# Kernel optimization log

Hardware: AMD Instinct MI355X
Metric: run time of the kernel (lower is better)

## Reference

```python
import jax, jax.numpy as jnp
import numpy as np

NUM_GROUPS = 32
EPS = 1e-6


def group_norm(x, gamma, beta):
    # x: [b, c, h, w]
    b, c, h, w = x.shape
    xg = x.reshape(b, NUM_GROUPS, c // NUM_GROUPS, h, w)
    mean = jnp.mean(xg, axis=(2, 3, 4), keepdims=True)
    var = jnp.var(xg, axis=(2, 3, 4), keepdims=True)
    xn = ((xg - mean) * jax.lax.rsqrt(var + EPS)).reshape(b, c, h, w)
    return xn * gamma[None, :, None, None] + beta[None, :, None, None]


def conv1x1(x, w, b):
    # 1x1 conv == channel-mixing linear: x [b,c,h,w], w [o,c], b [o]
    return jnp.einsum('bchw,oc->bohw', x, w) + b[None, :, None, None]


def setup_inputs() -> dict:
    key = jax.random.key(0)
    ks = jax.random.split(key, 11)
    B, C, H, W = 4, 512, 64, 64
    scale = 1.0 / np.sqrt(C)
    inp = {
        'x': jax.random.normal(ks[0], (B, C, H, W), jnp.float32),
        'gn_gamma': jnp.ones((C,), jnp.float32),
        'gn_beta': jnp.zeros((C,), jnp.float32),
        'wq': jax.random.normal(ks[1], (C, C), jnp.float32) * scale,
        'bq': jnp.zeros((C,), jnp.float32),
        'wk': jax.random.normal(ks[2], (C, C), jnp.float32) * scale,
        'bk': jnp.zeros((C,), jnp.float32),
        'wv': jax.random.normal(ks[3], (C, C), jnp.float32) * scale,
        'bv': jnp.zeros((C,), jnp.float32),
        'wo': jax.random.normal(ks[4], (C, C), jnp.float32) * scale,
        'bo': jnp.zeros((C,), jnp.float32),
    }
    return inp


def reference(x, gn_gamma, gn_beta, wq, bq, wk, bk, wv, bv, wo, bo):
    b, c, h, w = x.shape
    nx = group_norm(x, gn_gamma, gn_beta)
    q = conv1x1(nx, wq, bq).reshape(b, c, h * w)
    k = conv1x1(nx, wk, bk).reshape(b, c, h * w)
    v = conv1x1(nx, wv, bv).reshape(b, c, h * w)
    # score[b, i, j] = <q[:, i], k[:, j]> / sqrt(c); softmax over j (keys)
    score = jnp.einsum('bci,bcj->bij', q, k) / jnp.sqrt(jnp.asarray(c, x.dtype))
    score = jax.nn.softmax(score, axis=2)
    # out[b, c, i] = sum_j v[b, c, j] * score[b, i, j]
    out = jnp.einsum('bcj,bij->bci', v, score).reshape(b, c, h, w)
    out = conv1x1(out, wo, bo)
    return x + out
```

## Files before the change

kernel.cpp:

```cpp
#include <hip/hip_runtime.h>

#define B_   4
#define C_   512
#define G_   32
#define CPG  16
#define N_   4096

typedef unsigned short u16;
typedef __attribute__((ext_vector_type(4))) float f32x4;
typedef __attribute__((ext_vector_type(8))) short s16x8;
typedef __attribute__((ext_vector_type(8))) u16   u16x8;
typedef __attribute__((ext_vector_type(4))) u16   u16x4;

__device__ __forceinline__ u16 f2bf(float f) {
    union { float f; unsigned u; } x; x.f = f;
    unsigned r = x.u + 0x7fffu + ((x.u >> 16) & 1u);
    return (u16)(r >> 16);
}

__global__ __launch_bounds__(256)
void gn_part_kernel(const float* __restrict__ x, float2* __restrict__ partial)
{
    int blk = blockIdx.x;
    int bg = blk >> 3, s = blk & 7;
    const float* base = x + (size_t)bg * CPG * N_ + s * 8192;
    int t = threadIdx.x;

    float sm = 0.f, ss = 0.f;
    #pragma unroll
    for (int i = 0; i < 8192; i += 1024) {
        float4 v = *reinterpret_cast<const float4*>(base + i + t * 4);
        sm += v.x + v.y + v.z + v.w;
        ss += v.x * v.x + v.y * v.y + v.z * v.z + v.w * v.w;
    }
    __shared__ float rs[256], rss[256];
    rs[t] = sm; rss[t] = ss;
    __syncthreads();
    for (int off = 128; off > 0; off >>= 1) {
        if (t < off) { rs[t] += rs[t + off]; rss[t] += rss[t + off]; }
        __syncthreads();
    }
    if (t == 0) partial[blk] = make_float2(rs[0], rss[0]);
}

__global__ __launch_bounds__(256)
void gn_combine_kernel(const float2* __restrict__ partial,
                       const float* __restrict__ gamma,
                       const float* __restrict__ beta,
                       float* __restrict__ scale, float* __restrict__ shift)
{
    int bg = threadIdx.x;
    if (bg >= 128) return;
    int b = bg >> 5, g = bg & 31;
    float sm = 0.f, ss = 0.f;
    #pragma unroll
    for (int s = 0; s < 8; ++s) {
        float2 p = partial[bg * 8 + s];
        sm += p.x; ss += p.y;
    }
    const float inv_n = 1.f / 65536.f;
    float mean = sm * inv_n;
    float var  = ss * inv_n - mean * mean;
    float rstd = rsqrtf(var + 1e-6f);
    #pragma unroll
    for (int cc = 0; cc < CPG; ++cc) {
        int c = g * CPG + cc;
        float sc = gamma[c] * rstd;
        scale[b * C_ + c] = sc;
        shift[b * C_ + c] = beta[c] - mean * sc;
    }
}

__global__ __launch_bounds__(256)
void wcvt_kernel(const float* __restrict__ wq, const float* __restrict__ wk,
                 const float* __restrict__ wv, const float* __restrict__ wo,
                 u16* __restrict__ wqb, u16* __restrict__ wkb,
                 u16* __restrict__ wvb, u16* __restrict__ wob)
{
    int idx = (blockIdx.x * 256 + threadIdx.x) * 4;
    {
        float4 a = *reinterpret_cast<const float4*>(wq + idx);
        u16x4 r = { f2bf(a.x), f2bf(a.y), f2bf(a.z), f2bf(a.w) };
        *reinterpret_cast<u16x4*>(wqb + idx) = r;
    }
    {
        float4 a = *reinterpret_cast<const float4*>(wk + idx);
        u16x4 r = { f2bf(a.x), f2bf(a.y), f2bf(a.z), f2bf(a.w) };
        *reinterpret_cast<u16x4*>(wkb + idx) = r;
    }
    {
        float4 a = *reinterpret_cast<const float4*>(wv + idx);
        u16x4 r = { f2bf(a.x), f2bf(a.y), f2bf(a.z), f2bf(a.w) };
        *reinterpret_cast<u16x4*>(wvb + idx) = r;
    }
    {
        float4 a = *reinterpret_cast<const float4*>(wo + idx);
        u16x4 r = { f2bf(a.x), f2bf(a.y), f2bf(a.z), f2bf(a.w) };
        *reinterpret_cast<u16x4*>(wob + idx) = r;
    }
}

__global__ __launch_bounds__(256)
void nxt_kernel(const float* __restrict__ x, const float* __restrict__ scale,
                const float* __restrict__ shift, u16* __restrict__ nx_t)
{
    int b  = blockIdx.z;
    int n0 = blockIdx.x * 64, c0 = blockIdx.y * 64;
    const float* xb = x + ((size_t)b * C_ + c0) * N_ + n0;
    u16* ob = nx_t + ((size_t)b * N_ + n0) * C_ + c0;
    int t = threadIdx.x;
    int tx = t & 15, ty = t >> 4;

    __shared__ float tile[64][65];
    #pragma unroll
    for (int r = 0; r < 4; ++r) {
        int c = ty * 4 + r;
        float sc = scale[b * C_ + c0 + c];
        float sh = shift[b * C_ + c0 + c];
        float4 v = *reinterpret_cast<const float4*>(xb + (size_t)c * N_ + tx * 4);
        tile[c][tx * 4 + 0] = v.x * sc + sh;
        tile[c][tx * 4 + 1] = v.y * sc + sh;
        tile[c][tx * 4 + 2] = v.z * sc + sh;
        tile[c][tx * 4 + 3] = v.w * sc + sh;
    }
    __syncthreads();
    int nn = t >> 2, cc0 = (t & 3) * 16;
    u16x8 o0, o1;
    #pragma unroll
    for (int j = 0; j < 8; ++j) o0[j] = f2bf(tile[cc0 + j][nn]);
    #pragma unroll
    for (int j = 0; j < 8; ++j) o1[j] = f2bf(tile[cc0 + 8 + j][nn]);
    *reinterpret_cast<u16x8*>(ob + (size_t)nn * C_ + cc0)     = o0;
    *reinterpret_cast<u16x8*>(ob + (size_t)nn * C_ + cc0 + 8) = o1;
}

template<int BM, int BN, int EPI>
__device__ __forceinline__
void gemm_dev(int i0, int j0,
              const u16* __restrict__ A, const u16* __restrict__ B,
              void* __restrict__ Dp, const float* __restrict__ bias,
              const float* __restrict__ resid,
              int Nn, int K, int lda, int ldb, float scl,
              float* __restrict__ psum, const float* __restrict__ colsc)
{
    constexpr int WM = BM / 2, WN = BN / 2;
    constexpr int MI = WM / 16, NI = WN / 16;

    __shared__ u16 As[BM * 64];
    __shared__ u16 Bs[BN * 64];

    const int t  = threadIdx.x;
    const int l  = t & 63;
    const int w  = t >> 6;
    const int wr = w >> 1;
    const int wc = w & 1;

    const int srow = l >> 3;
    const int sgr  = ((l & 7) ^ (l >> 3)) * 8;

    const int fr = l & 15;
    const int q  = l >> 4;

    f32x4 acc[MI][NI];
    #pragma unroll
    for (int a = 0; a < MI; ++a)
        #pragma unroll
        for (int b2 = 0; b2 < NI; ++b2) acc[a][b2] = 0.f;

    for (int k0 = 0; k0 < K; k0 += 64) {
        #pragma unroll
        for (int r = 0; r < BM / 32; ++r) {
            int s = r * 4 + w;
            const u16* ga = A + (size_t)(i0 + s * 8 + srow) * lda + (k0 + sgr);
            __builtin_amdgcn_global_load_lds(
                (const __attribute__((address_space(1))) void*)ga,
                (__attribute__((address_space(3))) void*)&As[s * 512], 16, 0, 0);
        }
        #pragma unroll
        for (int r = 0; r < BN / 32; ++r) {
            int s = r * 4 + w;
            const u16* gb = B + (size_t)(j0 + s * 8 + srow) * ldb + (k0 + sgr);
            __builtin_amdgcn_global_load_lds(
                (const __attribute__((address_space(1))) void*)gb,
                (__attribute__((address_space(3))) void*)&Bs[s * 512], 16, 0, 0);
        }
        __syncthreads();

        #pragma unroll
        for (int h = 0; h < 2; ++h) {
            s16x8 af[MI], bfr[NI];
            #pragma unroll
            for (int mi = 0; mi < MI; ++mi) {
                int r = wr * WM + mi * 16 + fr;
                int p = (h * 4 + q) ^ (r & 7);
                af[mi] = *reinterpret_cast<const s16x8*>(&As[r * 64 + p * 8]);
            }
            #pragma unroll
            for (int ni = 0; ni < NI; ++ni) {
                int r = wc * WN + ni * 16 + fr;
                int p = (h * 4 + q) ^ (r & 7);
                bfr[ni] = *reinterpret_cast<const s16x8*>(&Bs[r * 64 + p * 8]);
            }
            #pragma unroll
            for (int mi = 0; mi < MI; ++mi)
                #pragma unroll
                for (int ni = 0; ni < NI; ++ni)
                    acc[mi][ni] = __builtin_amdgcn_mfma_f32_16x16x32_bf16(
                        af[mi], bfr[ni], acc[mi][ni], 0, 0, 0);
        }
        __syncthreads();
    }

    const int orow = (l >> 4) * 4;
    const int ocol = l & 15;

    if constexpr (EPI == 2) {
        __shared__ float sstl[2][2][64];
        u16* D = (u16*)Dp;
        #pragma unroll
        for (int mi = 0; mi < MI; ++mi) {
            int ib = i0 + wr * WM + mi * 16 + orow;
            float pr[4] = {0.f, 0.f, 0.f, 0.f};
            #pragma unroll
            for (int ni = 0; ni < NI; ++ni) {
                int jb = j0 + wc * WN + ni * 16 + ocol;
                #pragma unroll
                for (int e = 0; e < 4; ++e) {
                    float ex = __expf(acc[mi][ni][e] * scl);
                    D[(size_t)(ib + e) * Nn + jb] = f2bf(ex);
                    pr[e] += ex;
                }
            }
            #pragma unroll
            for (int e = 0; e < 4; ++e) {
                pr[e] += __shfl_xor(pr[e], 1);
                pr[e] += __shfl_xor(pr[e], 2);
                pr[e] += __shfl_xor(pr[e], 4);
                pr[e] += __shfl_xor(pr[e], 8);
            }
            if ((l & 15) == 0) {
                #pragma unroll
                for (int e = 0; e < 4; ++e)
                    sstl[wr][wc][mi * 16 + (l >> 4) * 4 + e] = pr[e];
            }
        }
        __syncthreads();
        if (t < 128) {
            int wr2 = t >> 6, r = t & 63;
            psum[i0 + wr2 * 64 + r] = sstl[wr2][0][r] + sstl[wr2][1][r];
        }
    } else {
        #pragma unroll
        for (int mi = 0; mi < MI; ++mi) {
            #pragma unroll
            for (int ni = 0; ni < NI; ++ni) {
                int ib = i0 + wr * WM + mi * 16 + orow;
                int jb = j0 + wc * WN + ni * 16 + ocol;
                if constexpr (EPI == 0 || EPI == 1 || EPI == 4) {
                    u16* D = (u16*)Dp;
                    float bj = 0.f;
                    if constexpr (EPI == 0) bj = bias[jb];
                    #pragma unroll
                    for (int e = 0; e < 4; ++e) {
                        float vv = acc[mi][ni][e];
                        if constexpr (EPI == 0) vv += bj;
                        if constexpr (EPI == 1) vv += bias[ib + e];
                        D[(size_t)(ib + e) * Nn + jb] = f2bf(vv);
                    }
                } else {
                    float* D = (float*)Dp;
                    float cs = colsc[jb];
                    #pragma unroll
                    for (int e = 0; e < 4; ++e)
                        D[(size_t)(ib + e) * Nn + jb] =
                            acc[mi][ni][e] * cs + bias[ib + e] + resid[(size_t)(ib + e) * Nn + jb];
                }
            }
        }
    }
}

__global__ __launch_bounds__(256)
void qk_gemm(const u16* __restrict__ nx_t, const u16* __restrict__ wqb,
             const u16* __restrict__ wkb, const float* __restrict__ bq,
             const float* __restrict__ bk, u16* __restrict__ q_t,
             u16* __restrict__ k_t)
{
    int z = blockIdx.z, b = z & 3, isk = z >> 2;
    gemm_dev<128, 128, 0>(blockIdx.y * 128, blockIdx.x * 128,
                          nx_t + (size_t)b * N_ * C_, isk ? wkb : wqb,
                          (isk ? k_t : q_t) + (size_t)b * N_ * C_,
                          isk ? bk : bq, nullptr, C_, C_, C_, C_, 1.f,
                          nullptr, nullptr);
}

__global__ __launch_bounds__(256)
void v_gemm(const u16* __restrict__ wvb, const u16* __restrict__ nx_t,
            const float* __restrict__ bv, u16* __restrict__ vbuf)
{
    int b = blockIdx.z;
    gemm_dev<128, 128, 1>(blockIdx.y * 128, blockIdx.x * 128,
                          wvb, nx_t + (size_t)b * N_ * C_, vbuf + (size_t)b * C_ * N_,
                          bv, nullptr, N_, C_, C_, C_, 1.f, nullptr, nullptr);
}

__global__ __launch_bounds__(256)
void scores_gemm(const u16* __restrict__ q_t, const u16* __restrict__ k_t,
                 u16* __restrict__ S_bf, float* __restrict__ psum)
{
    int b = blockIdx.z;
    float* ps = psum + ((size_t)b * 32 + blockIdx.x) * N_;
    gemm_dev<128, 128, 2>(blockIdx.y * 128, blockIdx.x * 128,
                          q_t + (size_t)b * N_ * C_, k_t + (size_t)b * N_ * C_,
                          S_bf + (size_t)b * N_ * N_, nullptr, nullptr, N_, C_, C_, C_,
                          0.044194173824159216f, ps, nullptr);
}

__global__ __launch_bounds__(256)
void lsum_kernel(const float* __restrict__ psum, float* __restrict__ inv_l)
{
    int r = blockIdx.x * 256 + threadIdx.x;
    int b = r >> 12, i = r & (N_ - 1);
    const float* p = psum + (size_t)b * 32 * N_ + i;
    float s = 0.f;
    #pragma unroll
    for (int jt = 0; jt < 32; ++jt) s += p[(size_t)jt * N_];
    inv_l[r] = 1.f / s;
}

__global__ __launch_bounds__(256)
void pv_part(const u16* __restrict__ S_bf, const u16* __restrict__ vbuf,
             u16* __restrict__ attn_t)
{
    int id  = blockIdx.x;
    int xcd = id & 7, slot = id >> 3;
    int yz  = xcd * 16 + (slot >> 3);
    int ct  = slot & 7;
    int it  = yz & 31, b = yz >> 5;
    const u16* Pb = S_bf + (size_t)b * N_ * N_;
    const u16* Vb = vbuf + (size_t)b * C_ * N_;
    u16*       Ob = attn_t + (size_t)b * N_ * C_;

    const int i0 = it * 128, c0 = ct * 64;
    const int t = threadIdx.x, l = t & 63, w = t >> 6;
    const int wr = w >> 1, wc = w & 1;
    const int srow = l >> 3;
    const int sgr  = ((l & 7) ^ (l >> 3)) * 8;
    const int fr = l & 15, q = l >> 4;

    __shared__ u16 As[128 * 64];
    __shared__ u16 Bs[64 * 64];

    f32x4 acc[4][2];
    #pragma unroll
    for (int a = 0; a < 4; ++a)
        #pragma unroll
        for (int b2 = 0; b2 < 2; ++b2) acc[a][b2] = 0.f;

    for (int k0 = 0; k0 < N_; k0 += 64) {
        #pragma unroll
        for (int r = 0; r < 4; ++r) {
            int s = r * 4 + w;
            const u16* ga = Pb + (size_t)(i0 + s * 8 + srow) * N_ + (k0 + sgr);
            __builtin_amdgcn_global_load_lds(
                (const __attribute__((address_space(1))) void*)ga,
                (__attribute__((address_space(3))) void*)&As[s * 512], 16, 0, 0);
        }
        #pragma unroll
        for (int r = 0; r < 2; ++r) {
            int s = r * 4 + w;
            const u16* gb = Vb + (size_t)(c0 + s * 8 + srow) * N_ + (k0 + sgr);
            __builtin_amdgcn_global_load_lds(
                (const __attribute__((address_space(1))) void*)gb,
                (__attribute__((address_space(3))) void*)&Bs[s * 512], 16, 0, 0);
        }
        __syncthreads();
        #pragma unroll
        for (int h = 0; h < 2; ++h) {
            s16x8 af[4], bfr[2];
            #pragma unroll
            for (int mi = 0; mi < 4; ++mi) {
                int r = wr * 64 + mi * 16 + fr;
                int p = (h * 4 + q) ^ (r & 7);
                af[mi] = *reinterpret_cast<const s16x8*>(&As[r * 64 + p * 8]);
            }
            #pragma unroll
            for (int ni = 0; ni < 2; ++ni) {
                int r = wc * 32 + ni * 16 + fr;
                int p = (h * 4 + q) ^ (r & 7);
                bfr[ni] = *reinterpret_cast<const s16x8*>(&Bs[r * 64 + p * 8]);
            }
            #pragma unroll
            for (int mi = 0; mi < 4; ++mi)
                #pragma unroll
                for (int ni = 0; ni < 2; ++ni)
                    acc[mi][ni] = __builtin_amdgcn_mfma_f32_16x16x32_bf16(
                        af[mi], bfr[ni], acc[mi][ni], 0, 0, 0);
        }
        __syncthreads();
    }

    const int orow = (l >> 4) * 4;
    const int ocol = l & 15;
    #pragma unroll
    for (int mi = 0; mi < 4; ++mi) {
        #pragma unroll
        for (int ni = 0; ni < 2; ++ni) {
            int ib = i0 + wr * 64 + mi * 16 + orow;
            int jb = c0 + wc * 32 + ni * 16 + ocol;
            #pragma unroll
            for (int e = 0; e < 4; ++e)
                Ob[(size_t)(ib + e) * C_ + jb] = f2bf(acc[mi][ni][e]);
        }
    }
}

__global__ __launch_bounds__(256)
void final_gemm(const u16* __restrict__ wob, const u16* __restrict__ attn_t,
                const float* __restrict__ bo, const float* __restrict__ x,
                const float* __restrict__ inv_l, float* __restrict__ outp)
{
    int b = blockIdx.z;
    gemm_dev<128, 128, 3>(blockIdx.y * 128, blockIdx.x * 128,
                          wob, attn_t + (size_t)b * N_ * C_, outp + (size_t)b * C_ * N_,
                          bo, x + (size_t)b * C_ * N_, N_, C_, C_, C_, 1.f,
                          nullptr, inv_l + (size_t)b * N_);
}

extern "C" void kernel_launch(void* const* d_in, const int* in_sizes, int n_in,
                              void* d_out, int out_size, void* d_ws, size_t ws_size,
                              hipStream_t stream)
{
    const float* x     = (const float*)d_in[0];
    const float* gamma = (const float*)d_in[1];
    const float* beta  = (const float*)d_in[2];
    const float* wq    = (const float*)d_in[3];
    const float* bq    = (const float*)d_in[4];
    const float* wk    = (const float*)d_in[5];
    const float* bk    = (const float*)d_in[6];
    const float* wv    = (const float*)d_in[7];
    const float* bv    = (const float*)d_in[8];
    const float* wo    = (const float*)d_in[9];
    const float* bo    = (const float*)d_in[10];
    float* out = (float*)d_out;

    char* p = (char*)d_ws;
    auto take = [&](size_t bytes) { char* r = p; p += (bytes + 255) & ~(size_t)255; return r; };
    float* scale = (float*)take(B_ * C_ * 4);
    float* shift = (float*)take(B_ * C_ * 4);
    float2* gpart = (float2*)take(1024 * 8);
    u16* wqb = (u16*)take((size_t)C_ * C_ * 2);
    u16* wkb = (u16*)take((size_t)C_ * C_ * 2);
    u16* wvb = (u16*)take((size_t)C_ * C_ * 2);
    u16* wob = (u16*)take((size_t)C_ * C_ * 2);
    u16* nx_t  = (u16*)take((size_t)B_ * N_ * C_ * 2);
    u16* q_t   = (u16*)take((size_t)B_ * N_ * C_ * 2);
    u16* k_t   = (u16*)take((size_t)B_ * N_ * C_ * 2);
    u16* vbuf  = (u16*)take((size_t)B_ * C_ * N_ * 2);
    float* psum  = (float*)take((size_t)B_ * 32 * N_ * 4);
    float* inv_l = (float*)take((size_t)B_ * N_ * 4);
    u16* S_bf = (u16*)take((size_t)B_ * N_ * N_ * 2);
    u16* attn_t = nx_t;

    gn_part_kernel<<<1024, 256, 0, stream>>>(x, gpart);
    gn_combine_kernel<<<1, 256, 0, stream>>>(gpart, gamma, beta, scale, shift);
    wcvt_kernel<<<256, 256, 0, stream>>>(wq, wk, wv, wo, wqb, wkb, wvb, wob);
    nxt_kernel<<<dim3(N_ / 64, C_ / 64, B_), 256, 0, stream>>>(x, scale, shift, nx_t);

    qk_gemm<<<dim3(C_ / 128, N_ / 128, 8), 256, 0, stream>>>(nx_t, wqb, wkb, bq, bk, q_t, k_t);
    v_gemm<<<dim3(N_ / 128, C_ / 128, B_), 256, 0, stream>>>(wvb, nx_t, bv, vbuf);

    scores_gemm<<<dim3(N_ / 128, N_ / 128, B_), 256, 0, stream>>>(q_t, k_t, S_bf, psum);
    lsum_kernel<<<B_ * N_ / 256, 256, 0, stream>>>(psum, inv_l);
    pv_part<<<1024, 256, 0, stream>>>(S_bf, vbuf, attn_t);

    final_gemm<<<dim3(N_ / 128, C_ / 128, B_), 256, 0, stream>>>(wob, attn_t, bo, x, inv_l, out);
}
```

Measured before the change: 260.8 us.

## Merge prep kernels and fuse Q/K/V projections into one launch

Merges the group-norm partial-sum kernel and the weight bf16 conversion into one launch, and folds the group-norm combine step into the transpose/normalize kernel, where each block recomputes its 64 channels' scale/shift into shared memory. The Q/K and V projection GEMMs are also merged into one grid with 12 z-slices, and the Q/K block indexing is remapped to match the new grid. This cuts the launch count from six to three and lets the V GEMM blocks run alongside the Q/K blocks, at the cost of redundant per-block combine work.

```diff
diff --git a/kernel.cpp b/kernel.cpp
--- a/kernel.cpp
+++ b/kernel.cpp
@@ -19,90 +19,61 @@
 }
 
 __global__ __launch_bounds__(256)
-void gn_part_kernel(const float* __restrict__ x, float2* __restrict__ partial)
-{
-    int blk = blockIdx.x;
-    int bg = blk >> 3, s = blk & 7;
-    const float* base = x + (size_t)bg * CPG * N_ + s * 8192;
-    int t = threadIdx.x;
-
-    float sm = 0.f, ss = 0.f;
-    #pragma unroll
-    for (int i = 0; i < 8192; i += 1024) {
-        float4 v = *reinterpret_cast<const float4*>(base + i + t * 4);
-        sm += v.x + v.y + v.z + v.w;
-        ss += v.x * v.x + v.y * v.y + v.z * v.z + v.w * v.w;
-    }
-    __shared__ float rs[256], rss[256];
-    rs[t] = sm; rss[t] = ss;
-    __syncthreads();
-    for (int off = 128; off > 0; off >>= 1) {
-        if (t < off) { rs[t] += rs[t + off]; rss[t] += rss[t + off]; }
-        __syncthreads();
-    }
-    if (t == 0) partial[blk] = make_float2(rs[0], rss[0]);
-}
-
-__global__ __launch_bounds__(256)
-void gn_combine_kernel(const float2* __restrict__ partial,
-                       const float* __restrict__ gamma,
-                       const float* __restrict__ beta,
-                       float* __restrict__ scale, float* __restrict__ shift)
-{
-    int bg = threadIdx.x;
-    if (bg >= 128) return;
-    int b = bg >> 5, g = bg & 31;
-    float sm = 0.f, ss = 0.f;
-    #pragma unroll
-    for (int s = 0; s < 8; ++s) {
-        float2 p = partial[bg * 8 + s];
-        sm += p.x; ss += p.y;
-    }
-    const float inv_n = 1.f / 65536.f;
-    float mean = sm * inv_n;
-    float var  = ss * inv_n - mean * mean;
-    float rstd = rsqrtf(var + 1e-6f);
-    #pragma unroll
-    for (int cc = 0; cc < CPG; ++cc) {
-        int c = g * CPG + cc;
-        float sc = gamma[c] * rstd;
-        scale[b * C_ + c] = sc;
-        shift[b * C_ + c] = beta[c] - mean * sc;
-    }
-}
-
-__global__ __launch_bounds__(256)
-void wcvt_kernel(const float* __restrict__ wq, const float* __restrict__ wk,
+void prep_kernel(const float* __restrict__ x, float2* __restrict__ gpart,
+                 const float* __restrict__ wq, const float* __restrict__ wk,
                  const float* __restrict__ wv, const float* __restrict__ wo,
                  u16* __restrict__ wqb, u16* __restrict__ wkb,
                  u16* __restrict__ wvb, u16* __restrict__ wob)
 {
-    int idx = (blockIdx.x * 256 + threadIdx.x) * 4;
-    {
-        float4 a = *reinterpret_cast<const float4*>(wq + idx);
-        u16x4 r = { f2bf(a.x), f2bf(a.y), f2bf(a.z), f2bf(a.w) };
-        *reinterpret_cast<u16x4*>(wqb + idx) = r;
-    }
-    {
-        float4 a = *reinterpret_cast<const float4*>(wk + idx);
-        u16x4 r = { f2bf(a.x), f2bf(a.y), f2bf(a.z), f2bf(a.w) };
-        *reinterpret_cast<u16x4*>(wkb + idx) = r;
-    }
-    {
-        float4 a = *reinterpret_cast<const float4*>(wv + idx);
-        u16x4 r = { f2bf(a.x), f2bf(a.y), f2bf(a.z), f2bf(a.w) };
-        *reinterpret_cast<u16x4*>(wvb + idx) = r;
-    }
-    {
-        float4 a = *reinterpret_cast<const float4*>(wo + idx);
-        u16x4 r = { f2bf(a.x), f2bf(a.y), f2bf(a.z), f2bf(a.w) };
-        *reinterpret_cast<u16x4*>(wob + idx) = r;
-    }
-}
-
-__global__ __launch_bounds__(256)
-void nxt_kernel(const float* __restrict__ x, const float* __restrict__ scale,
-                const float* __restrict__ shift, u16* __restrict__ nx_t)
+    int blk = blockIdx.x;
+    int t = threadIdx.x;
+    if (blk < 1024) {
+        int bg = blk >> 3, s = blk & 7;
+        const float* base = x + (size_t)bg * CPG * N_ + s * 8192;
+        float sm = 0.f, ss = 0.f;
+        #pragma unroll
+        for (int i = 0; i < 8192; i += 1024) {
+            float4 v = *reinterpret_cast<const float4*>(base + i + t * 4);
+            sm += v.x + v.y + v.z + v.w;
+            ss += v.x * v.x + v.y * v.y + v.z * v.z + v.w * v.w;
+        }
+        __shared__ float rs[256], rss[256];
+        rs[t] = sm; rss[t] = ss;
+        __syncthreads();
+        for (int off = 128; off > 0; off >>= 1) {
+            if (t < off) { rs[t] += rs[t + off]; rss[t] += rss[t + off]; }
+            __syncthreads();
+        }
+        if (t == 0) gpart[blk] = make_float2(rs[0], rss[0]);
+    } else {
+        int idx = ((blk - 1024) * 256 + t) * 4;
+        {
+            float4 a = *reinterpret_cast<const float4*>(wq + idx);
+            u16x4 r = { f2bf(a.x), f2bf(a.y), f2bf(a.z), f2bf(a.w) };
+            *reinterpret_cast<u16x4*>(wqb + idx) = r;
+        }
+        {
+            float4 a = *reinterpret_cast<const float4*>(wk + idx);
+            u16x4 r = { f2bf(a.x), f2bf(a.y), f2bf(a.z), f2bf(a.w) };
+            *reinterpret_cast<u16x4*>(wkb + idx) = r;
+        }
+        {
+            float4 a = *reinterpret_cast<const float4*>(wv + idx);
+            u16x4 r = { f2bf(a.x), f2bf(a.y), f2bf(a.z), f2bf(a.w) };
+            *reinterpret_cast<u16x4*>(wvb + idx) = r;
+        }
+        {
+            float4 a = *reinterpret_cast<const float4*>(wo + idx);
+            u16x4 r = { f2bf(a.x), f2bf(a.y), f2bf(a.z), f2bf(a.w) };
+            *reinterpret_cast<u16x4*>(wob + idx) = r;
+        }
+    }
+}
+
+__global__ __launch_bounds__(256)
+void nxt_kernel(const float* __restrict__ x, const float2* __restrict__ gpart,
+                const float* __restrict__ gamma, const float* __restrict__ beta,
+                u16* __restrict__ nx_t)
 {
     int b  = blockIdx.z;
     int n0 = blockIdx.x * 64, c0 = blockIdx.y * 64;
@@ -111,12 +82,32 @@
     int t = threadIdx.x;
     int tx = t & 15, ty = t >> 4;
 
+    __shared__ float scale_s[64], shift_s[64];
+    if (t < 64) {
+        int c = c0 + t;
+        int bg = b * G_ + (c >> 4);
+        float sm = 0.f, ss = 0.f;
+        #pragma unroll
+        for (int s = 0; s < 8; ++s) {
+            float2 p2 = gpart[bg * 8 + s];
+            sm += p2.x; ss += p2.y;
+        }
+        const float inv_n = 1.f / 65536.f;
+        float mean = sm * inv_n;
+        float var  = ss * inv_n - mean * mean;
+        float rstd = rsqrtf(var + 1e-6f);
+        float sc = gamma[c] * rstd;
+        scale_s[t] = sc;
+        shift_s[t] = beta[c] - mean * sc;
+    }
+    __syncthreads();
+
     __shared__ float tile[64][65];
     #pragma unroll
     for (int r = 0; r < 4; ++r) {
         int c = ty * 4 + r;
-        float sc = scale[b * C_ + c0 + c];
-        float sh = shift[b * C_ + c0 + c];
+        float sc = scale_s[c];
+        float sh = shift_s[c];
         float4 v = *reinterpret_cast<const float4*>(xb + (size_t)c * N_ + tx * 4);
         tile[c][tx * 4 + 0] = v.x * sc + sh;
         tile[c][tx * 4 + 1] = v.y * sc + sh;
@@ -281,27 +272,27 @@
 }
 
 __global__ __launch_bounds__(256)
-void qk_gemm(const u16* __restrict__ nx_t, const u16* __restrict__ wqb,
-             const u16* __restrict__ wkb, const float* __restrict__ bq,
-             const float* __restrict__ bk, u16* __restrict__ q_t,
-             u16* __restrict__ k_t)
-{
-    int z = blockIdx.z, b = z & 3, isk = z >> 2;
-    gemm_dev<128, 128, 0>(blockIdx.y * 128, blockIdx.x * 128,
-                          nx_t + (size_t)b * N_ * C_, isk ? wkb : wqb,
-                          (isk ? k_t : q_t) + (size_t)b * N_ * C_,
-                          isk ? bk : bq, nullptr, C_, C_, C_, C_, 1.f,
-                          nullptr, nullptr);
-}
-
-__global__ __launch_bounds__(256)
-void v_gemm(const u16* __restrict__ wvb, const u16* __restrict__ nx_t,
-            const float* __restrict__ bv, u16* __restrict__ vbuf)
-{
-    int b = blockIdx.z;
-    gemm_dev<128, 128, 1>(blockIdx.y * 128, blockIdx.x * 128,
-                          wvb, nx_t + (size_t)b * N_ * C_, vbuf + (size_t)b * C_ * N_,
-                          bv, nullptr, N_, C_, C_, C_, 1.f, nullptr, nullptr);
+void qkv_gemm(const u16* __restrict__ nx_t, const u16* __restrict__ wqb,
+              const u16* __restrict__ wkb, const u16* __restrict__ wvb,
+              const float* __restrict__ bq, const float* __restrict__ bk,
+              const float* __restrict__ bv, u16* __restrict__ q_t,
+              u16* __restrict__ k_t, u16* __restrict__ vbuf)
+{
+    int z = blockIdx.z;
+    if (z < 8) {
+        int b = z & 3, isk = z >> 2;
+        gemm_dev<128, 128, 0>(blockIdx.x * 128, blockIdx.y * 128,
+                              nx_t + (size_t)b * N_ * C_, isk ? wkb : wqb,
+                              (isk ? k_t : q_t) + (size_t)b * N_ * C_,
+                              isk ? bk : bq, nullptr, C_, C_, C_, C_, 1.f,
+                              nullptr, nullptr);
+    } else {
+        int b = z - 8;
+        gemm_dev<128, 128, 1>(blockIdx.y * 128, blockIdx.x * 128,
+                              wvb, nx_t + (size_t)b * N_ * C_,
+                              vbuf + (size_t)b * C_ * N_,
+                              bv, nullptr, N_, C_, C_, C_, 1.f, nullptr, nullptr);
+    }
 }
 
 __global__ __launch_bounds__(256)
@@ -446,8 +437,6 @@
 
     char* p = (char*)d_ws;
     auto take = [&](size_t bytes) { char* r = p; p += (bytes + 255) & ~(size_t)255; return r; };
-    float* scale = (float*)take(B_ * C_ * 4);
-    float* shift = (float*)take(B_ * C_ * 4);
     float2* gpart = (float2*)take(1024 * 8);
     u16* wqb = (u16*)take((size_t)C_ * C_ * 2);
     u16* wkb = (u16*)take((size_t)C_ * C_ * 2);
@@ -462,13 +451,13 @@
     u16* S_bf = (u16*)take((size_t)B_ * N_ * N_ * 2);
     u16* attn_t = nx_t;
 
-    gn_part_kernel<<<1024, 256, 0, stream>>>(x, gpart);
-    gn_combine_kernel<<<1, 256, 0, stream>>>(gpart, gamma, beta, scale, shift);
-    wcvt_kernel<<<256, 256, 0, stream>>>(wq, wk, wv, wo, wqb, wkb, wvb, wob);
-    nxt_kernel<<<dim3(N_ / 64, C_ / 64, B_), 256, 0, stream>>>(x, scale, shift, nx_t);
-
-    qk_gemm<<<dim3(C_ / 128, N_ / 128, 8), 256, 0, stream>>>(nx_t, wqb, wkb, bq, bk, q_t, k_t);
-    v_gemm<<<dim3(N_ / 128, C_ / 128, B_), 256, 0, stream>>>(wvb, nx_t, bv, vbuf);
+    prep_kernel<<<1280, 256, 0, stream>>>(x, gpart, wq, wk, wv, wo,
+                                          wqb, wkb, wvb, wob);
+    nxt_kernel<<<dim3(N_ / 64, C_ / 64, B_), 256, 0, stream>>>(
+        x, gpart, gamma, beta, nx_t);
+
+    qkv_gemm<<<dim3(32, 4, 12), 256, 0, stream>>>(
+        nx_t, wqb, wkb, wvb, bq, bk, bv, q_t, k_t, vbuf);
 
     scores_gemm<<<dim3(N_ / 128, N_ / 128, B_), 256, 0, stream>>>(q_t, k_t, S_bf, psum);
     lsum_kernel<<<B_ * N_ / 256, 256, 0, stream>>>(psum, inv_l);
```

Measured after the change: 271.2 us. 1.04x slower.
